# Performance work log

Hardware: AMD Instinct MI355X
Metric: run time of the kernel (lower is better)

Reference implementation:

```python
import jax, jax.numpy as jnp
import numpy as np

TOP_K = 2  # num_experts_per_tok


def setup_inputs() -> dict:
    key = jax.random.key(0)
    k1, k2, k3, k4, k5 = jax.random.split(key, 5)
    B, S, D, F, E = 2, 1024, 1024, 2048, 8
    return {
        "x": jax.random.normal(k1, (B, S, D), dtype=jnp.float32),
        "router_kernel_DE": jax.random.normal(k2, (D, E), dtype=jnp.float32) * 0.02,
        "kernel_gating_EDF": jax.random.normal(k3, (E, D, F), dtype=jnp.float32) * 0.02,
        "kernel_up_EDF": jax.random.normal(k4, (E, D, F), dtype=jnp.float32) * 0.02,
        "kernel_down_EFD": jax.random.normal(k5, (E, F, D), dtype=jnp.float32) * 0.02,
    }


def reference(x, router_kernel_DE, kernel_gating_EDF, kernel_up_EDF, kernel_down_EFD):
    E = router_kernel_DE.shape[-1]
    x = x.astype(jnp.float32)
    # --- Router ---
    logits_BSE = jnp.einsum('BSD,DE->BSE', x, router_kernel_DE)
    probs_BSE = jax.nn.softmax(logits_BSE.astype(jnp.float32), axis=-1)
    weights_BSK, indices_BSK = jax.lax.top_k(probs_BSE, TOP_K)
    norm_weights_BSK = jax.nn.softmax(weights_BSK, axis=-1)
    # scatter top-k weights into dense [B,S,E]
    one_hot_BSKE = jax.nn.one_hot(indices_BSK, num_classes=E, dtype=x.dtype)
    full_weights_BSE = jnp.sum(one_hot_BSKE * norm_weights_BSK[..., None], axis=2)
    # --- Dense-over-all-experts MoE forward ---
    gating_BSEF = jnp.einsum('BSD,EDF->BSEF', x, kernel_gating_EDF)
    act_BSEF = jax.nn.silu(gating_BSEF)
    up_BSEF = jnp.einsum('BSD,EDF->BSEF', x, kernel_up_EDF)
    fuse_BSEF = act_BSEF * up_BSEF
    down_BSED = jnp.einsum('BSEF,EFD->BSED', fuse_BSEF, kernel_down_EFD)
    out_BSD = jnp.einsum('BSED,BSE->BSD', down_BSED, full_weights_BSE)
    return out_BSD.astype(jnp.float32)
```

## Files before the change

### kernel.cpp

```cpp
#include <hip/hip_runtime.h>
#include <hip/hip_bf16.h>
#include <stdint.h>

#define T_TOK 2048
#define DIM 1024
#define FDIM 2048
#define NEXP 8
#define NSLOT 4096

typedef short bf16x8 __attribute__((ext_vector_type(8)));
typedef unsigned short u16x8 __attribute__((ext_vector_type(8)));
typedef float f32x4 __attribute__((ext_vector_type(4)));

__device__ __forceinline__ unsigned short f2bf(float f) {
  union { float f; unsigned int u; } v; v.f = f;
  unsigned int r = v.u + 0x7FFFu + ((v.u >> 16) & 1u);
  return (unsigned short)(r >> 16);
}

__device__ __forceinline__ float bf2f(unsigned short x) {
  union { unsigned int u; float f; } v; v.u = ((unsigned int)x) << 16;
  return v.f;
}

__device__ __forceinline__ void gld_lds16(const void* g, void* l) {
  __builtin_amdgcn_global_load_lds(
      (const __attribute__((address_space(1))) unsigned int*)g,
      (__attribute__((address_space(3))) unsigned int*)l, 16, 0, 0);
}

__global__ void router_kernel(const float* __restrict__ x, const float* __restrict__ rk,
                              int* __restrict__ counts, int* __restrict__ tok_e,
                              float* __restrict__ tok_w, unsigned short* __restrict__ xb) {
  int w = threadIdx.x >> 6, lane = threadIdx.x & 63;
  int t = blockIdx.x * 4 + w;
  float acc[NEXP];
#pragma unroll
  for (int e = 0; e < NEXP; ++e) acc[e] = 0.f;
  const float4* xr = (const float4*)(x + (size_t)t * DIM);
#pragma unroll
  for (int i = 0; i < 4; ++i) {
    float4 xv = xr[i * 64 + lane];
    uint2 pk;
    pk.x = ((unsigned)f2bf(xv.y) << 16) | f2bf(xv.x);
    pk.y = ((unsigned)f2bf(xv.w) << 16) | f2bf(xv.z);
    *(uint2*)(xb + (size_t)t * DIM + (i * 64 + lane) * 4) = pk;
    int d0 = (i * 64 + lane) * 4;
#pragma unroll
    for (int j = 0; j < 4; ++j) {
      const float4* rr = (const float4*)(rk + (size_t)(d0 + j) * NEXP);
      float4 r0 = rr[0], r1 = rr[1];
      float xs = (j == 0) ? xv.x : (j == 1) ? xv.y : (j == 2) ? xv.z : xv.w;
      acc[0] += xs * r0.x; acc[1] += xs * r0.y; acc[2] += xs * r0.z; acc[3] += xs * r0.w;
      acc[4] += xs * r1.x; acc[5] += xs * r1.y; acc[6] += xs * r1.z; acc[7] += xs * r1.w;
    }
  }
#pragma unroll
  for (int off = 32; off > 0; off >>= 1) {
#pragma unroll
    for (int e = 0; e < NEXP; ++e) acc[e] += __shfl_xor(acc[e], off, 64);
  }
  if (lane == 0) {
    float m = acc[0];
    for (int e = 1; e < NEXP; ++e) m = fmaxf(m, acc[e]);
    float p[NEXP], s = 0.f;
    for (int e = 0; e < NEXP; ++e) { p[e] = expf(acc[e] - m); s += p[e]; }
    float inv = 1.f / s;
    for (int e = 0; e < NEXP; ++e) p[e] *= inv;
    int i1 = 0;
    for (int e = 1; e < NEXP; ++e) if (p[e] > p[i1]) i1 = e;
    int i2 = (i1 == 0) ? 1 : 0;
    for (int e = 0; e < NEXP; ++e) if (e != i1 && p[e] > p[i2]) i2 = e;
    float e1 = expf(p[i1]), e2 = expf(p[i2]);
    float winv = 1.f / (e1 + e2);
    tok_e[t * 2] = i1; tok_e[t * 2 + 1] = i2;
    tok_w[t * 2] = e1 * winv; tok_w[t * 2 + 1] = e2 * winv;
    atomicAdd(&counts[i1], 1); atomicAdd(&counts[i2], 1);
  }
}

__global__ void assign_kernel(const int* __restrict__ tok_e, const float* __restrict__ tok_w,
                              const int* __restrict__ counts, int* __restrict__ cursor,
                              int* __restrict__ slot_token, float* __restrict__ slot_weight,
                              int* __restrict__ tok_slot) {
  int t = blockIdx.x * 256 + threadIdx.x;
  if (t >= T_TOK) return;
#pragma unroll
  for (int k = 0; k < 2; ++k) {
    int e = tok_e[t * 2 + k];
    int off = 0;
#pragma unroll
    for (int j = 0; j < NEXP; ++j) off += (j < e) ? counts[j] : 0;
    int pos = atomicAdd(&cursor[e], 1);
    int slot = off + pos;
    slot_token[slot] = t;
    slot_weight[slot] = tok_w[t * 2 + k];
    tok_slot[t * 2 + k] = slot;
  }
}

__global__ void transpose_all(const float* __restrict__ wg_f, const float* __restrict__ wu_f,
                              const float* __restrict__ wd_f, unsigned short* __restrict__ wgt,
                              unsigned short* __restrict__ wut, unsigned short* __restrict__ wdt) {
  __shared__ float lds[64][65];
  int bid = blockIdx.x, e = blockIdx.y;
  const float* in;
  unsigned short* out;
  int R, C, rb, cb;
  if (bid < 1024) {
    in = (bid < 512) ? wg_f : wu_f;
    out = (bid < 512) ? wgt : wut;
    int id = bid & 511;
    R = DIM; C = FDIM;
    cb = (id & 31) * 64; rb = (id >> 5) * 64;
  } else {
    in = wd_f; out = wdt;
    int id = bid - 1024;
    R = FDIM; C = DIM;
    cb = (id & 15) * 64; rb = (id >> 4) * 64;
  }
  size_t base = (size_t)e * (size_t)R * (size_t)C;
  int tid = threadIdx.x;
  int col4 = (tid & 15) * 4, row = tid >> 4;
#pragma unroll
  for (int it = 0; it < 4; ++it) {
    int r = row + it * 16;
    float4 v = *(const float4*)(in + base + (size_t)(rb + r) * C + cb + col4);
    lds[col4 + 0][r] = v.x; lds[col4 + 1][r] = v.y;
    lds[col4 + 2][r] = v.z; lds[col4 + 3][r] = v.w;
  }
  __syncthreads();
  int r8 = (tid & 7) * 8, c = tid >> 3;
#pragma unroll
  for (int it = 0; it < 2; ++it) {
    int cc = c + it * 32;
    uint4 v;
    v.x = ((unsigned)f2bf(lds[cc][r8 + 1]) << 16) | f2bf(lds[cc][r8 + 0]);
    v.y = ((unsigned)f2bf(lds[cc][r8 + 3]) << 16) | f2bf(lds[cc][r8 + 2]);
    v.z = ((unsigned)f2bf(lds[cc][r8 + 5]) << 16) | f2bf(lds[cc][r8 + 4]);
    v.w = ((unsigned)f2bf(lds[cc][r8 + 7]) << 16) | f2bf(lds[cc][r8 + 6]);
    *(uint4*)(out + base + (size_t)(cb + cc) * R + rb + r8) = v;
  }
}

__device__ __forceinline__ bool tile_decode(const int* counts, int ys, int& e, int& mt,
                                            int& off, int& cnt) {
  mt = ys; off = 0;
  for (e = 0; e < NEXP; ++e) {
    cnt = counts[e];
    int ntl = (cnt + 127) >> 7;
    if (mt < ntl) return true;
    mt -= ntl; off += cnt;
  }
  return false;
}

__global__ __launch_bounds__(256) void gemm_gateup(
    const unsigned short* __restrict__ xb, const unsigned short* __restrict__ wg,
    const unsigned short* __restrict__ wu, const int* __restrict__ counts,
    const int* __restrict__ slot_token, unsigned short* __restrict__ fuse) {
  int e, mt, off, cnt;
  if (!tile_decode(counts, blockIdx.y, e, mt, off, cnt)) return;
  int nt = blockIdx.x;
  __shared__ unsigned short Al[2][128 * 64];
  __shared__ unsigned short Bgl[2][64 * 64];
  __shared__ unsigned short Bul[2][64 * 64];
  int tid = threadIdx.x, w = tid >> 6, lane = tid & 63;
  int csrc = ((lane & 7) ^ (lane >> 3)) * 8;
  unsigned aoff[4];
  unsigned boff[2];
#pragma unroll
  for (int ii = 0; ii < 4; ++ii) {
    int r = (w * 4 + ii) * 8 + (lane >> 3);
    int row = mt * 128 + r;
    int tok = (row < cnt) ? slot_token[off + row] : 0;
    aoff[ii] = (unsigned)(tok * DIM + csrc);
  }
#pragma unroll
  for (int ii = 0; ii < 2; ++ii) {
    int r = (w * 2 + ii) * 8 + (lane >> 3);
    boff[ii] = (unsigned)((e * FDIM + nt * 64 + r) * DIM + csrc);
  }
  f32x4 accg[4][2] = {};
  f32x4 accu[4][2] = {};
  int wr = (w >> 1) * 64, wc = (w & 1) * 32;
  int swz = (lane & 7) << 3;
  int kof0 = ((lane >> 4) * 8) ^ swz;
  int kof1 = (32 + (lane >> 4) * 8) ^ swz;

  auto stage = [&](int buf, int k0) {
#pragma unroll
    for (int ii = 0; ii < 4; ++ii)
      gld_lds16(xb + aoff[ii] + k0, &Al[buf][(w * 4 + ii) * 512]);
#pragma unroll
    for (int ii = 0; ii < 2; ++ii) {
      gld_lds16(wg + boff[ii] + k0, &Bgl[buf][(w * 2 + ii) * 512]);
      gld_lds16(wu + boff[ii] + k0, &Bul[buf][(w * 2 + ii) * 512]);
    }
  };
  auto compute = [&](int buf) {
#pragma unroll
    for (int kk = 0; kk < 2; ++kk) {
      int kof = kk ? kof1 : kof0;
      bf16x8 af[4], bg[2], bu[2];
#pragma unroll
      for (int q = 0; q < 4; ++q)
        af[q] = *(const bf16x8*)&Al[buf][(wr + q * 16 + (lane & 15)) * 64 + kof];
#pragma unroll
      for (int q = 0; q < 2; ++q) {
        bg[q] = *(const bf16x8*)&Bgl[buf][(wc + q * 16 + (lane & 15)) * 64 + kof];
        bu[q] = *(const bf16x8*)&Bul[buf][(wc + q * 16 + (lane & 15)) * 64 + kof];
      }
#pragma unroll
      for (int m4 = 0; m4 < 4; ++m4) {
#pragma unroll
        for (int n4 = 0; n4 < 2; ++n4) {
          accg[m4][n4] = __builtin_amdgcn_mfma_f32_16x16x32_bf16(af[m4], bg[n4], accg[m4][n4], 0, 0, 0);
          accu[m4][n4] = __builtin_amdgcn_mfma_f32_16x16x32_bf16(af[m4], bu[n4], accu[m4][n4], 0, 0, 0);
        }
      }
    }
  };

  stage(0, 0);
  asm volatile("s_waitcnt vmcnt(0)" ::: "memory");
  __builtin_amdgcn_s_barrier();
  int cb = 0;
  for (int k0 = 0; k0 < DIM; k0 += 64) {
    if (k0 + 64 < DIM) stage(cb ^ 1, k0 + 64);
    __builtin_amdgcn_sched_barrier(0);
    compute(cb);
    __builtin_amdgcn_sched_barrier(0);
    asm volatile("s_waitcnt vmcnt(0)" ::: "memory");
    __builtin_amdgcn_s_barrier();
    cb ^= 1;
  }

#pragma unroll
  for (int m4 = 0; m4 < 4; ++m4) {
#pragma unroll
    for (int n4 = 0; n4 < 2; ++n4) {
      f32x4 g = accg[m4][n4], u = accu[m4][n4];
#pragma unroll
      for (int j = 0; j < 4; ++j) {
        int r = wr + m4 * 16 + (lane >> 4) * 4 + j;
        int row = mt * 128 + r;
        if (row < cnt) {
          float gv = g[j];
          float val = gv / (1.f + expf(-gv)) * u[j];
          int f = nt * 64 + wc + n4 * 16 + (lane & 15);
          fuse[(size_t)(off + row) * FDIM + f] = f2bf(val);
        }
      }
    }
  }
}

__global__ __launch_bounds__(256) void gemm_down(
    const unsigned short* __restrict__ fuse, const unsigned short* __restrict__ wd,
    const int* __restrict__ counts, const float* __restrict__ slot_weight,
    unsigned short* __restrict__ part4) {
  int e, mt, off, cnt;
  if (!tile_decode(counts, blockIdx.y, e, mt, off, cnt)) return;
  int nt = blockIdx.x;
  int z = blockIdx.z;
  int kbase = z * (FDIM / 4);
  __shared__ unsigned short Al[128 * 64];
  __shared__ unsigned short Bl[128 * 64];
  int tid = threadIdx.x, w = tid >> 6, lane = tid & 63;
  int csrc = ((lane & 7) ^ (lane >> 3)) * 8;
  unsigned aoff[4];
  unsigned boff[4];
#pragma unroll
  for (int ii = 0; ii < 4; ++ii) {
    int r = (w * 4 + ii) * 8 + (lane >> 3);
    int row = mt * 128 + r;
    int grow = (row < cnt) ? (off + row) : off;
    aoff[ii] = (unsigned)(grow * FDIM + kbase + csrc);
    boff[ii] = (unsigned)((e * DIM + nt * 128 + r) * FDIM + kbase + csrc);
  }
  f32x4 acc[4][4] = {};
  int wr = (w >> 1) * 64, wc = (w & 1) * 64;
  int swz = (lane & 7) << 3;
  int kof0 = ((lane >> 4) * 8) ^ swz;
  int kof1 = (32 + (lane >> 4) * 8) ^ swz;
  for (int k0 = 0; k0 < FDIM / 4; k0 += 64) {
#pragma unroll
    for (int ii = 0; ii < 4; ++ii) {
      gld_lds16(fuse + aoff[ii] + k0, &Al[(w * 4 + ii) * 512]);
      gld_lds16(wd + boff[ii] + k0, &Bl[(w * 4 + ii) * 512]);
    }
    __syncthreads();
#pragma unroll
    for (int kk = 0; kk < 2; ++kk) {
      int kof = kk ? kof1 : kof0;
      bf16x8 af[4], bfr[4];
#pragma unroll
      for (int q = 0; q < 4; ++q) {
        af[q] = *(const bf16x8*)&Al[(wr + q * 16 + (lane & 15)) * 64 + kof];
        bfr[q] = *(const bf16x8*)&Bl[(wc + q * 16 + (lane & 15)) * 64 + kof];
      }
#pragma unroll
      for (int m4 = 0; m4 < 4; ++m4) {
#pragma unroll
        for (int n4 = 0; n4 < 4; ++n4) {
          acc[m4][n4] = __builtin_amdgcn_mfma_f32_16x16x32_bf16(af[m4], bfr[n4], acc[m4][n4], 0, 0, 0);
        }
      }
    }
    __syncthreads();
  }
#pragma unroll
  for (int m4 = 0; m4 < 4; ++m4) {
#pragma unroll
    for (int j = 0; j < 4; ++j) {
      int r = wr + m4 * 16 + (lane >> 4) * 4 + j;
      int row = mt * 128 + r;
      if (row < cnt) {
        float wgt = slot_weight[off + row];
#pragma unroll
        for (int n4 = 0; n4 < 4; ++n4) {
          int d = nt * 128 + wc + n4 * 16 + (lane & 15);
          part4[((size_t)z * NSLOT + off + row) * DIM + d] = f2bf(acc[m4][n4][j] * wgt);
        }
      }
    }
  }
}

__global__ void combine_kernel(const unsigned short* __restrict__ part4,
                               const int* __restrict__ tok_slot, float* __restrict__ out) {
  int i = blockIdx.x * 256 + threadIdx.x;
  int t = i >> 7;
  int c = i & 127;
  int s0 = tok_slot[t * 2], s1 = tok_slot[t * 2 + 1];
  const u16x8* base = (const u16x8*)part4;
  float o[8];
#pragma unroll
  for (int j = 0; j < 8; ++j) o[j] = 0.f;
#pragma unroll
  for (int z = 0; z < 4; ++z) {
    u16x8 a = base[((size_t)z * NSLOT + s0) * (DIM / 8) + c];
    u16x8 b = base[((size_t)z * NSLOT + s1) * (DIM / 8) + c];
#pragma unroll
    for (int j = 0; j < 8; ++j) o[j] += bf2f(a[j]) + bf2f(b[j]);
  }
  float4* dst = (float4*)(out + (size_t)t * DIM + c * 8);
  dst[0] = make_float4(o[0], o[1], o[2], o[3]);
  dst[1] = make_float4(o[4], o[5], o[6], o[7]);
}

extern "C" void kernel_launch(void* const* d_in, const int* in_sizes, int n_in,
                              void* d_out, int out_size, void* d_ws, size_t ws_size,
                              hipStream_t stream) {
  (void)in_sizes; (void)n_in; (void)out_size;
  const float* x    = (const float*)d_in[0];
  const float* rk   = (const float*)d_in[1];
  const float* wg_f = (const float*)d_in[2];
  const float* wu_f = (const float*)d_in[3];
  const float* wd_f = (const float*)d_in[4];
  float* out = (float*)d_out;

  char* ws = (char*)d_ws;
  size_t o_xb   = 0;
  size_t o_wg   = o_xb + (size_t)T_TOK * DIM * 2;
  size_t o_wu   = o_wg + (size_t)NEXP * FDIM * DIM * 2;
  size_t o_wd   = o_wu + (size_t)NEXP * FDIM * DIM * 2;
  size_t o_fuse = o_wd + (size_t)NEXP * DIM * FDIM * 2;
  size_t o_meta = o_fuse + (size_t)NSLOT * FDIM * 2;
  size_t o_counts = o_meta;
  size_t o_cursor = o_counts + 32;
  size_t o_tok_e  = o_cursor + 32;
  size_t o_tok_w  = o_tok_e + (size_t)T_TOK * 2 * 4;
  size_t o_tok_s  = o_tok_w + (size_t)T_TOK * 2 * 4;
  size_t o_st     = o_tok_s + (size_t)T_TOK * 2 * 4;
  size_t o_sw     = o_st + (size_t)NSLOT * 4;
  size_t need     = o_sw + (size_t)NSLOT * 4;
  if (ws_size < need) return;

  unsigned short* xb    = (unsigned short*)(ws + o_xb);
  unsigned short* wgt   = (unsigned short*)(ws + o_wg);
  unsigned short* wut   = (unsigned short*)(ws + o_wu);
  unsigned short* wdt   = (unsigned short*)(ws + o_wd);
  unsigned short* fuse  = (unsigned short*)(ws + o_fuse);
  unsigned short* part4 = (unsigned short*)(ws + o_wg);
  int* counts          = (int*)(ws + o_counts);
  int* cursor          = (int*)(ws + o_cursor);
  int* tok_e           = (int*)(ws + o_tok_e);
  float* tok_w         = (float*)(ws + o_tok_w);
  int* tok_slot        = (int*)(ws + o_tok_s);
  int* slot_token      = (int*)(ws + o_st);
  float* slot_weight   = (float*)(ws + o_sw);

  hipMemsetAsync(ws + o_counts, 0, 64, stream);
  router_kernel<<<T_TOK / 4, 256, 0, stream>>>(x, rk, counts, tok_e, tok_w, xb);
  assign_kernel<<<T_TOK / 256, 256, 0, stream>>>(tok_e, tok_w, counts, cursor,
                                                 slot_token, slot_weight, tok_slot);
  transpose_all<<<dim3(1536, NEXP), 256, 0, stream>>>(wg_f, wu_f, wd_f, wgt, wut, wdt);
  gemm_gateup<<<dim3(FDIM / 64, 40, 1), 256, 0, stream>>>(xb, wgt, wut, counts,
                                                          slot_token, fuse);
  gemm_down<<<dim3(DIM / 128, 40, 4), 256, 0, stream>>>(fuse, wdt, counts,
                                                        slot_weight, part4);
  combine_kernel<<<(T_TOK * DIM / 8) / 256, 256, 0, stream>>>(part4, tok_slot, out);
}
```

Measured before the change: 244.8 us.

## Single-buffer A tiles and double-buffer weight tiles with partial vmcnt waits

In the gate/up GEMM, the A (token) tile drops to a single LDS buffer and is loaded after compute, while weight tiles stay double-buffered and are prefetched one step ahead using a partial vmcnt wait. The down GEMM, which previously loaded synchronously with __syncthreads, gets the same scheme with a double-buffered B tile. The aim is to overlap the weight-tile global loads with MFMA compute and, in gate/up, to reduce LDS use so more blocks can be resident. The trade-off is that the A-tile load is now exposed after each compute step, and the pipeline relies on exact vmcnt accounting.

```diff
diff --git a/kernel.cpp b/kernel.cpp
--- a/kernel.cpp
+++ b/kernel.cpp
@@ -162,7 +162,7 @@
   int e, mt, off, cnt;
   if (!tile_decode(counts, blockIdx.y, e, mt, off, cnt)) return;
   int nt = blockIdx.x;
-  __shared__ unsigned short Al[2][128 * 64];
+  __shared__ unsigned short Al[128 * 64];
   __shared__ unsigned short Bgl[2][64 * 64];
   __shared__ unsigned short Bul[2][64 * 64];
   int tid = threadIdx.x, w = tid >> 6, lane = tid & 63;
@@ -188,10 +188,12 @@
   int kof0 = ((lane >> 4) * 8) ^ swz;
   int kof1 = (32 + (lane >> 4) * 8) ^ swz;
 
-  auto stage = [&](int buf, int k0) {
+  auto stage_A = [&](int k0) {
 #pragma unroll
     for (int ii = 0; ii < 4; ++ii)
-      gld_lds16(xb + aoff[ii] + k0, &Al[buf][(w * 4 + ii) * 512]);
+      gld_lds16(xb + aoff[ii] + k0, &Al[(w * 4 + ii) * 512]);
+  };
+  auto stage_B = [&](int buf, int k0) {
 #pragma unroll
     for (int ii = 0; ii < 2; ++ii) {
       gld_lds16(wg + boff[ii] + k0, &Bgl[buf][(w * 2 + ii) * 512]);
@@ -205,7 +207,7 @@
       bf16x8 af[4], bg[2], bu[2];
 #pragma unroll
       for (int q = 0; q < 4; ++q)
-        af[q] = *(const bf16x8*)&Al[buf][(wr + q * 16 + (lane & 15)) * 64 + kof];
+        af[q] = *(const bf16x8*)&Al[(wr + q * 16 + (lane & 15)) * 64 + kof];
 #pragma unroll
       for (int q = 0; q < 2; ++q) {
         bg[q] = *(const bf16x8*)&Bgl[buf][(wc + q * 16 + (lane & 15)) * 64 + kof];
@@ -222,17 +224,25 @@
     }
   };
 
-  stage(0, 0);
+  stage_B(0, 0);
+  stage_A(0);
   asm volatile("s_waitcnt vmcnt(0)" ::: "memory");
   __builtin_amdgcn_s_barrier();
   int cb = 0;
-  for (int k0 = 0; k0 < DIM; k0 += 64) {
-    if (k0 + 64 < DIM) stage(cb ^ 1, k0 + 64);
+  for (int t = 0; t < 16; ++t) {
+    if (t < 15) {
+      stage_B(cb ^ 1, (t + 1) * 64);
+      __builtin_amdgcn_sched_barrier(0);
+      asm volatile("s_waitcnt vmcnt(4)" ::: "memory");
+    } else {
+      asm volatile("s_waitcnt vmcnt(0)" ::: "memory");
+    }
+    __builtin_amdgcn_s_barrier();
     __builtin_amdgcn_sched_barrier(0);
     compute(cb);
     __builtin_amdgcn_sched_barrier(0);
-    asm volatile("s_waitcnt vmcnt(0)" ::: "memory");
     __builtin_amdgcn_s_barrier();
+    if (t < 15) stage_A((t + 1) * 64);
     cb ^= 1;
   }
 
@@ -266,7 +276,7 @@
   int z = blockIdx.z;
   int kbase = z * (FDIM / 4);
   __shared__ unsigned short Al[128 * 64];
-  __shared__ unsigned short Bl[128 * 64];
+  __shared__ unsigned short Bl[2][128 * 64];
   int tid = threadIdx.x, w = tid >> 6, lane = tid & 63;
   int csrc = ((lane & 7) ^ (lane >> 3)) * 8;
   unsigned aoff[4];
@@ -284,13 +294,18 @@
   int swz = (lane & 7) << 3;
   int kof0 = ((lane >> 4) * 8) ^ swz;
   int kof1 = (32 + (lane >> 4) * 8) ^ swz;
-  for (int k0 = 0; k0 < FDIM / 4; k0 += 64) {
-#pragma unroll
-    for (int ii = 0; ii < 4; ++ii) {
+
+  auto stage_A = [&](int k0) {
+#pragma unroll
+    for (int ii = 0; ii < 4; ++ii)
       gld_lds16(fuse + aoff[ii] + k0, &Al[(w * 4 + ii) * 512]);
-      gld_lds16(wd + boff[ii] + k0, &Bl[(w * 4 + ii) * 512]);
-    }
-    __syncthreads();
+  };
+  auto stage_B = [&](int buf, int k0) {
+#pragma unroll
+    for (int ii = 0; ii < 4; ++ii)
+      gld_lds16(wd + boff[ii] + k0, &Bl[buf][(w * 4 + ii) * 512]);
+  };
+  auto compute = [&](int buf) {
 #pragma unroll
     for (int kk = 0; kk < 2; ++kk) {
       int kof = kk ? kof1 : kof0;
@@ -298,7 +313,7 @@
 #pragma unroll
       for (int q = 0; q < 4; ++q) {
         af[q] = *(const bf16x8*)&Al[(wr + q * 16 + (lane & 15)) * 64 + kof];
-        bfr[q] = *(const bf16x8*)&Bl[(wc + q * 16 + (lane & 15)) * 64 + kof];
+        bfr[q] = *(const bf16x8*)&Bl[buf][(wc + q * 16 + (lane & 15)) * 64 + kof];
       }
 #pragma unroll
       for (int m4 = 0; m4 < 4; ++m4) {
@@ -308,8 +323,30 @@
         }
       }
     }
-    __syncthreads();
-  }
+  };
+
+  stage_B(0, 0);
+  stage_A(0);
+  asm volatile("s_waitcnt vmcnt(0)" ::: "memory");
+  __builtin_amdgcn_s_barrier();
+  int cb = 0;
+  for (int t = 0; t < 8; ++t) {
+    if (t < 7) {
+      stage_B(cb ^ 1, (t + 1) * 64);
+      __builtin_amdgcn_sched_barrier(0);
+      asm volatile("s_waitcnt vmcnt(4)" ::: "memory");
+    } else {
+      asm volatile("s_waitcnt vmcnt(0)" ::: "memory");
+    }
+    __builtin_amdgcn_s_barrier();
+    __builtin_amdgcn_sched_barrier(0);
+    compute(cb);
+    __builtin_amdgcn_sched_barrier(0);
+    __builtin_amdgcn_s_barrier();
+    if (t < 7) stage_A((t + 1) * 64);
+    cb ^= 1;
+  }
+
 #pragma unroll
   for (int m4 = 0; m4 < 4; ++m4) {
 #pragma unroll
```

New measurement: 243.6 us. No clear change (-0.5%).
